# Kernel optimization log

Hardware: AMD Instinct MI355X
Metric: run time of the kernel (lower is better)

Reference implementation:

```python
import jax, jax.numpy as jnp
import numpy as np

DN = ('NCHW', 'OIHW', 'NCHW')

def conv(x, w, b=None, pad=0):
    y = jax.lax.conv_general_dilated(x, w, (1, 1), [(pad, pad), (pad, pad)], dimension_numbers=DN)
    if b is not None:
        y = y + b[None, :, None, None]
    return y

def bn(x, g, b):
    # inference-mode BatchNorm with running_mean=0, running_var=1 (affine only)
    return g[None, :, None, None] * x + b[None, :, None, None]

def gru(msg, h, wg, bg, wc, g, be):
    gates = conv(jnp.concatenate([msg, h], axis=1), wg, bg)  # [B,2,H,W]
    r = jax.nn.sigmoid(gates[:, 0:1])
    u = jax.nn.sigmoid(gates[:, 1:2])
    cnm = jax.nn.leaky_relu(bn(conv(jnp.concatenate([msg, r * h], axis=1), wc), g, be), 0.01)
    return (1.0 - u) * h + u * cnm

def setup_inputs() -> dict:
    key = jax.random.key(0)
    ks = jax.random.split(key, 32)
    B, C, H, W = 8, 10, 192, 192
    s = 0.1
    inp = {
        'f_nodes': jax.random.normal(ks[0], (2, B, C, H, W), jnp.float32),
        'h_nodes': jax.random.normal(ks[1], (3, B, C, H, W), jnp.float32),
        'p_nodes': jax.random.normal(ks[2], (7, B, C, H, W), jnp.float32),
        'xh': jax.random.normal(ks[3], (B, C, H, W), jnp.float32),
        # Decomp_att: 1x1 conv 30->3
        'w_dmap': jax.random.normal(ks[4], (3, 30, 1, 1)) * s,
        'b_dmap': jnp.zeros((3,)),
        # Decomposition relation (shared across 2 children): 3x3 conv 20->10 + BN
        'w_decomp': jax.random.normal(ks[5], (10, 20, 3, 3)) * s,
        'g_decomp': jnp.ones((10,)), 'be_decomp': jnp.zeros((10,)),
        # Comp_att upper: 1x1 conv 40->1 ; lower: 20->1
        'w_cau': jax.random.normal(ks[6], (1, 40, 1, 1)) * s, 'b_cau': jnp.zeros((1,)),
        'w_cal': jax.random.normal(ks[7], (1, 20, 1, 1)) * s, 'b_cal': jnp.zeros((1,)),
        # Composition relation (shared across parts): 3x3 conv 20->10 + BN
        'w_cu': jax.random.normal(ks[8], (10, 20, 3, 3)) * s,
        'g_cu': jnp.ones((10,)), 'be_cu': jnp.zeros((10,)),
        'w_cl': jax.random.normal(ks[9], (10, 20, 3, 3)) * s,
        'g_cl': jnp.ones((10,)), 'be_cl': jnp.zeros((10,)),
        # ConvGRU upper: gates 1x1 20->2, candidate 1x1 20->10 + ABN(leaky_relu)
        'wg_u': jax.random.normal(ks[10], (2, 20, 1, 1)) * s, 'bg_u': jnp.zeros((2,)),
        'wc_u': jax.random.normal(ks[11], (10, 20, 1, 1)) * s,
        'g_u': jnp.ones((10,)), 'be_u': jnp.zeros((10,)),
        # ConvGRU lower
        'wg_l': jax.random.normal(ks[12], (2, 20, 1, 1)) * s, 'bg_l': jnp.zeros((2,)),
        'wc_l': jax.random.normal(ks[13], (10, 20, 1, 1)) * s,
        'g_l': jnp.ones((10,)), 'be_l': jnp.zeros((10,)),
    }
    return inp

def reference(f_nodes, h_nodes, p_nodes, xh,
              w_dmap, b_dmap, w_decomp, g_decomp, be_decomp,
              w_cau, b_cau, w_cal, b_cal,
              w_cu, g_cu, be_cu, w_cl, g_cl, be_cl,
              wg_u, bg_u, wc_u, g_u, be_u,
              wg_l, bg_l, wc_l, g_l, be_l):
    f1 = f_nodes[1]
    h1, h2 = h_nodes[1], h_nodes[2]

    # Decomp_att: 1x1 conv over [f1, h1, h2]
    decomp_map = conv(jnp.concatenate([f1, h1, h2], axis=1), w_dmap, b_dmap)  # [B,3,H,W]
    att = jax.nn.softmax(decomp_map, axis=1)

    # Decomposition (channels 0 is parent-self slot; children use slots 1,2)
    d0 = jax.nn.relu(bn(conv(jnp.concatenate([f1 * att[:, 1:2], h1], axis=1), w_decomp, pad=1), g_decomp, be_decomp))
    d1 = jax.nn.relu(bn(conv(jnp.concatenate([f1 * att[:, 2:3], h2], axis=1), w_decomp, pad=1), g_decomp, be_decomp))

    # Upper half: parts 1..4
    upper = [p_nodes[i] for i in (1, 2, 3, 4)]
    comp_map_u = jax.nn.sigmoid(conv(jnp.concatenate(upper, axis=1), w_cau, b_cau))  # [B,1,H,W]
    comp_u = sum(jax.nn.relu(bn(conv(jnp.concatenate([h1, c * comp_map_u], axis=1), w_cu, pad=1), g_cu, be_cu)) for c in upper)
    msg_u = d0 + comp_u
    xh_u = gru(msg_u, h1, wg_u, bg_u, wc_u, g_u, be_u)

    # Lower half: parts 5..6
    lower = [p_nodes[i] for i in (5, 6)]
    comp_map_l = jax.nn.sigmoid(conv(jnp.concatenate(lower, axis=1), w_cal, b_cal))
    comp_l = sum(jax.nn.relu(bn(conv(jnp.concatenate([h2, c * comp_map_l], axis=1), w_cl, pad=1), g_cl, be_cl)) for c in lower)
    msg_l = d1 + comp_l
    xh_l = gru(msg_l, h2, wg_l, bg_l, wc_l, g_l, be_l)

    xh_new = jnp.stack([h_nodes[0], xh_u, xh_l], axis=0)  # [3,B,10,H,W]
    return (xh_new, decomp_map, comp_map_u, comp_map_l)
```

## Files before the change

### kernel.cpp

```cpp
#include <hip/hip_runtime.h>

#define HW 36864
#define WD 192
#define BB 8
#define CC 10

typedef __attribute__((ext_vector_type(8))) short short8;
typedef __attribute__((ext_vector_type(4))) float f32x4;

__device__ __forceinline__ short f2bf(float v) {
    unsigned u = __float_as_uint(v);
    unsigned r = (u + 0x7fffu + ((u >> 16) & 1u)) >> 16;
    return (short)r;
}

__global__ __launch_bounds__(256) void maps_kernel(
    const float* __restrict__ f_nodes, const float* __restrict__ h_nodes,
    const float* __restrict__ p_nodes,
    const float* __restrict__ w_dmap, const float* __restrict__ b_dmap,
    const float* __restrict__ w_cau, const float* __restrict__ b_cau,
    const float* __restrict__ w_cal, const float* __restrict__ b_cal,
    float* __restrict__ out)
{
    int px = blockIdx.x * 256 + threadIdx.x;
    int b  = px / HW;
    int sp = px - b * HW;

    const float* f1 = f_nodes + (size_t)(1*BB + b)*CC*HW + sp;
    const float* h0 = h_nodes + (size_t)(0*BB + b)*CC*HW + sp;
    const float* h1 = h_nodes + (size_t)(1*BB + b)*CC*HW + sp;
    const float* h2 = h_nodes + (size_t)(2*BB + b)*CC*HW + sp;

    float fv[10], h1v[10], h2v[10];
    #pragma unroll
    for (int c = 0; c < 10; ++c) {
        fv[c]  = f1[(size_t)c*HW];
        h1v[c] = h1[(size_t)c*HW];
        h2v[c] = h2[(size_t)c*HW];
    }

    const size_t O1 = (size_t)3*BB*CC*HW;
    #pragma unroll
    for (int j = 0; j < 3; ++j) {
        float s = b_dmap[j];
        #pragma unroll
        for (int c = 0; c < 10; ++c) s = fmaf(w_dmap[j*30 + c],      fv[c],  s);
        #pragma unroll
        for (int c = 0; c < 10; ++c) s = fmaf(w_dmap[j*30 + 10 + c], h1v[c], s);
        #pragma unroll
        for (int c = 0; c < 10; ++c) s = fmaf(w_dmap[j*30 + 20 + c], h2v[c], s);
        out[O1 + ((size_t)b*3 + j)*HW + sp] = s;
    }

    float su = b_cau[0];
    #pragma unroll
    for (int i = 0; i < 4; ++i) {
        const float* p = p_nodes + (size_t)((1+i)*BB + b)*CC*HW + sp;
        #pragma unroll
        for (int c = 0; c < 10; ++c) su = fmaf(w_cau[i*10 + c], p[(size_t)c*HW], su);
    }
    const size_t O2 = O1 + (size_t)BB*3*HW;
    out[O2 + (size_t)b*HW + sp] = 1.f / (1.f + expf(-su));

    float sl = b_cal[0];
    #pragma unroll
    for (int i = 0; i < 2; ++i) {
        const float* p = p_nodes + (size_t)((5+i)*BB + b)*CC*HW + sp;
        #pragma unroll
        for (int c = 0; c < 10; ++c) sl = fmaf(w_cal[i*10 + c], p[(size_t)c*HW], sl);
    }
    const size_t O3 = O2 + (size_t)BB*HW;
    out[O3 + (size_t)b*HW + sp] = 1.f / (1.f + expf(-sl));

    float* o0 = out + (size_t)b*CC*HW + sp;
    #pragma unroll
    for (int c = 0; c < 10; ++c) o0[(size_t)c*HW] = h0[(size_t)c*HW];
}

__global__ __launch_bounds__(256) void half_kernel(
    const float* __restrict__ f1base,
    const float* __restrict__ hbase,
    const float* __restrict__ pbase, int nparts,
    const float* __restrict__ dmap, int attIdx,
    const float* __restrict__ cmap,
    const float* __restrict__ w_dec,
    const float* __restrict__ gD, const float* __restrict__ bD,
    const float* __restrict__ w_cmp,
    const float* __restrict__ gC, const float* __restrict__ bC,
    const float* __restrict__ wg, const float* __restrict__ bg,
    const float* __restrict__ wc, const float* __restrict__ gG,
    const float* __restrict__ beG,
    float* __restrict__ outp)
{
    __shared__ short sT[342*24];
    __shared__ short sWb[2*16*232];
    __shared__ float sMap[324];
    __shared__ float sMsg[256*12];
    __shared__ float sPar[302];

    const int tid  = threadIdx.x;
    const int lane = tid & 63;
    const int w    = tid >> 6;
    const int g    = lane >> 4;
    const int n    = lane & 15;
    const int b    = blockIdx.z;
    const int x0   = blockIdx.x*16, y0 = blockIdx.y*16;

    {
        int* z = (int*)sT;
        for (int i = tid; i < 342*24/2; i += 256) z[i] = 0;
        int* z2 = (int*)sWb;
        for (int i = tid; i < 2*16*232/2; i += 256) z2[i] = 0;
    }
    __syncthreads();

    for (int i = tid; i < 1800; i += 256) {
        int o = i/180, r = i - o*180;
        int ci = r/9, kp = r - ci*9;
        int slot_d = (ci >= 10) ? (ci - 10) : (ci + 10);
        sWb[o*232 + kp*24 + slot_d]      = f2bf(w_dec[i]);
        sWb[16*232 + o*232 + kp*24 + ci] = f2bf(w_cmp[i]);
    }
    if (tid < 10) {
        sPar[tid]    = gD[tid];  sPar[10+tid] = bD[tid];
        sPar[20+tid] = gC[tid];  sPar[30+tid] = bC[tid];
        sPar[40+tid] = gG[tid];  sPar[50+tid] = beG[tid];
    }
    if (tid < 40) sPar[60+tid]  = wg[tid];
    if (tid < 2)  sPar[100+tid] = bg[tid];
    if (tid >= 56 && tid < 256) sPar[102+(tid-56)] = (tid-56 < 200) ? wc[tid-56] : 0.f;

    for (int r = tid; r < 324; r += 256) {
        int yy = r/18, xx = r - yy*18;
        int gy = y0 + yy - 1, gx = x0 + xx - 1;
        float a = 0.f;
        if ((unsigned)gy < 192u && (unsigned)gx < 192u) {
            const float* dmb = dmap + (size_t)b*3*HW + gy*WD + gx;
            float d0 = dmb[0], d1 = dmb[HW], d2 = dmb[2*HW];
            float mx = fmaxf(d0, fmaxf(d1, d2));
            float e0 = expf(d0-mx), e1 = expf(d1-mx), e2 = expf(d2-mx);
            a = ((attIdx == 1) ? e1 : e2) / (e0 + e1 + e2);
        }
        sMap[r] = a;
    }
    __syncthreads();

    const float* fb = f1base + (size_t)b*CC*HW;
    const float* hb = hbase  + (size_t)b*CC*HW;
    for (int e = tid; e < 3240; e += 256) {
        int c = e/324, r = e - c*324;
        int yy = r/18, xx = r - yy*18;
        int gy = y0 + yy - 1, gx = x0 + xx - 1;
        float vh = 0.f, vf = 0.f;
        if ((unsigned)gy < 192u && (unsigned)gx < 192u) {
            int off = gy*WD + gx;
            vh = hb[(size_t)c*HW + off];
            vf = fb[(size_t)c*HW + off] * sMap[r];
        }
        sT[r*24 + c]      = f2bf(vh);
        sT[r*24 + 10 + c] = f2bf(vf);
    }
    __syncthreads();

    int aoff[7];
    #pragma unroll
    for (int t = 0; t < 7; ++t) {
        int ks = 32*t + 8*g;
        int kp = ks/24;
        int c8 = ks - kp*24;
        int ky = kp/3, kx = kp - ky*3;
        aoff[t] = ((ky*18) + kx + n)*24 + c8;
    }
    const int wbase = w*4*432;

    f32x4 msgf[4];
    {
        short8 bfr[7];
        #pragma unroll
        for (int t = 0; t < 7; ++t)
            bfr[t] = *(const short8*)(sWb + n*232 + 32*t + 8*g);
        f32x4 acc[4];
        #pragma unroll
        for (int mt = 0; mt < 4; ++mt) acc[mt] = (f32x4){0.f,0.f,0.f,0.f};
        #pragma unroll
        for (int t = 0; t < 7; ++t) {
            #pragma unroll
            for (int mt = 0; mt < 4; ++mt) {
                short8 a = *(const short8*)(sT + wbase + mt*432 + aoff[t]);
                acc[mt] = __builtin_amdgcn_mfma_f32_16x16x32_bf16(a, bfr[t], acc[mt], 0, 0, 0);
            }
        }
        int np = (n < 10) ? n : 9;
        float gDv = sPar[np], bDv = sPar[10+np];
        #pragma unroll
        for (int mt = 0; mt < 4; ++mt) {
            #pragma unroll
            for (int j = 0; j < 4; ++j)
                msgf[mt][j] = fmaxf(fmaf(gDv, acc[mt][j], bDv), 0.f);
        }
    }

    for (int r = tid; r < 324; r += 256) {
        int yy = r/18, xx = r - yy*18;
        int gy = y0 + yy - 1, gx = x0 + xx - 1;
        float a = 0.f;
        if ((unsigned)gy < 192u && (unsigned)gx < 192u)
            a = cmap[(size_t)b*HW + gy*WD + gx];
        sMap[r] = a;
    }

    short8 bfc[7];
    #pragma unroll
    for (int t = 0; t < 7; ++t)
        bfc[t] = *(const short8*)(sWb + 16*232 + n*232 + 32*t + 8*g);

    int np = (n < 10) ? n : 9;
    float gCv = sPar[20+np], bCv = sPar[30+np];
    __syncthreads();

    for (int j = 0; j < nparts; ++j) {
        const float* pb = pbase + ((size_t)j*BB + b)*CC*HW;
        for (int e = tid; e < 3240; e += 256) {
            int c = e/324, r = e - c*324;
            int yy = r/18, xx = r - yy*18;
            int gy = y0 + yy - 1, gx = x0 + xx - 1;
            float v = 0.f;
            if ((unsigned)gy < 192u && (unsigned)gx < 192u)
                v = pb[(size_t)c*HW + gy*WD + gx] * sMap[r];
            sT[r*24 + 10 + c] = f2bf(v);
        }
        __syncthreads();

        f32x4 acc[4];
        #pragma unroll
        for (int mt = 0; mt < 4; ++mt) acc[mt] = (f32x4){0.f,0.f,0.f,0.f};
        #pragma unroll
        for (int t = 0; t < 7; ++t) {
            #pragma unroll
            for (int mt = 0; mt < 4; ++mt) {
                short8 a = *(const short8*)(sT + wbase + mt*432 + aoff[t]);
                acc[mt] = __builtin_amdgcn_mfma_f32_16x16x32_bf16(a, bfc[t], acc[mt], 0, 0, 0);
            }
        }
        #pragma unroll
        for (int mt = 0; mt < 4; ++mt) {
            #pragma unroll
            for (int jj = 0; jj < 4; ++jj)
                msgf[mt][jj] += fmaxf(fmaf(gCv, acc[mt][jj], bCv), 0.f);
        }
        __syncthreads();
    }

    if (n < 10) {
        #pragma unroll
        for (int mt = 0; mt < 4; ++mt) {
            #pragma unroll
            for (int r2 = 0; r2 < 4; ++r2) {
                int q = (4*w + mt)*16 + 4*g + r2;
                sMsg[q*12 + n] = msgf[mt][r2];
            }
        }
    }
    __syncthreads();

    {
        int q = tid;
        int row = q >> 4, xx = q & 15;
        int gy = y0 + row, gx = x0 + xx;

        float msg[10], hc[10];
        #pragma unroll
        for (int c = 0; c < 10; ++c) msg[c] = sMsg[q*12 + c];
        const float* hp = hb + gy*WD + gx;
        #pragma unroll
        for (int c = 0; c < 10; ++c) hc[c] = hp[(size_t)c*HW];

        float g0 = sPar[100], g1 = sPar[101];
        #pragma unroll
        for (int c = 0; c < 10; ++c) {
            g0 = fmaf(sPar[60+c], msg[c], g0);
            g1 = fmaf(sPar[80+c], msg[c], g1);
        }
        #pragma unroll
        for (int c = 0; c < 10; ++c) {
            g0 = fmaf(sPar[70+c], hc[c], g0);
            g1 = fmaf(sPar[90+c], hc[c], g1);
        }
        float r = 1.f / (1.f + expf(-g0));
        float u = 1.f / (1.f + expf(-g1));

        float* op = outp + (size_t)b*CC*HW + gy*WD + gx;
        #pragma unroll
        for (int o = 0; o < 10; ++o) {
            float s = 0.f;
            const float* wr = &sPar[102 + o*20];
            #pragma unroll
            for (int c = 0; c < 10; ++c) s = fmaf(wr[c], msg[c], s);
            #pragma unroll
            for (int c = 0; c < 10; ++c) s = fmaf(wr[10+c], r*hc[c], s);
            s = fmaf(sPar[40+o], s, sPar[50+o]);
            s = (s > 0.f) ? s : 0.01f*s;
            op[(size_t)o*HW] = (1.f - u)*hc[o] + u*s;
        }
    }
}

extern "C" void kernel_launch(void* const* d_in, const int* in_sizes, int n_in,
                              void* d_out, int out_size, void* d_ws, size_t ws_size,
                              hipStream_t stream)
{
    const float* f_nodes = (const float*)d_in[0];
    const float* h_nodes = (const float*)d_in[1];
    const float* p_nodes = (const float*)d_in[2];
    const float* w_dmap   = (const float*)d_in[4];
    const float* b_dmap   = (const float*)d_in[5];
    const float* w_decomp = (const float*)d_in[6];
    const float* g_decomp = (const float*)d_in[7];
    const float* be_decomp= (const float*)d_in[8];
    const float* w_cau    = (const float*)d_in[9];
    const float* b_cau    = (const float*)d_in[10];
    const float* w_cal    = (const float*)d_in[11];
    const float* b_cal    = (const float*)d_in[12];
    const float* w_cu     = (const float*)d_in[13];
    const float* g_cu     = (const float*)d_in[14];
    const float* be_cu    = (const float*)d_in[15];
    const float* w_cl     = (const float*)d_in[16];
    const float* g_cl     = (const float*)d_in[17];
    const float* be_cl    = (const float*)d_in[18];
    const float* wg_u     = (const float*)d_in[19];
    const float* bg_u     = (const float*)d_in[20];
    const float* wc_u     = (const float*)d_in[21];
    const float* g_u      = (const float*)d_in[22];
    const float* be_u     = (const float*)d_in[23];
    const float* wg_l     = (const float*)d_in[24];
    const float* bg_l     = (const float*)d_in[25];
    const float* wc_l     = (const float*)d_in[26];
    const float* g_l      = (const float*)d_in[27];
    const float* be_l     = (const float*)d_in[28];

    float* out = (float*)d_out;
    const size_t O1 = (size_t)3*BB*CC*HW;
    const size_t O2 = O1 + (size_t)BB*3*HW;
    const size_t O3 = O2 + (size_t)BB*HW;

    maps_kernel<<<dim3((BB*HW)/256), dim3(256), 0, stream>>>(
        f_nodes, h_nodes, p_nodes, w_dmap, b_dmap, w_cau, b_cau, w_cal, b_cal, out);

    dim3 grid(WD/16, WD/16, BB), blk(256, 1, 1);

    half_kernel<<<grid, blk, 0, stream>>>(
        f_nodes + (size_t)1*BB*CC*HW,
        h_nodes + (size_t)1*BB*CC*HW,
        p_nodes + (size_t)1*BB*CC*HW, 4,
        out + O1, 1, out + O2,
        w_decomp, g_decomp, be_decomp,
        w_cu, g_cu, be_cu,
        wg_u, bg_u, wc_u, g_u, be_u,
        out + (size_t)1*BB*CC*HW);

    half_kernel<<<grid, blk, 0, stream>>>(
        f_nodes + (size_t)1*BB*CC*HW,
        h_nodes + (size_t)2*BB*CC*HW,
        p_nodes + (size_t)5*BB*CC*HW, 2,
        out + O1, 2, out + O3,
        w_decomp, g_decomp, be_decomp,
        w_cl, g_cl, be_cl,
        wg_l, bg_l, wc_l, g_l, be_l,
        out + (size_t)2*BB*CC*HW);
}
```

Baseline: 371.8 us.

## Precompute padded bf16 channel-last workspace and async-DMA tiles into merged half kernel

A prep kernel now computes the attention maps and the softmax/sigmoid scaling. It writes h, the scaled f and the scaled part tensors into a zero-padded bf16 channel-last workspace with 16-channel pixels. The half kernel serves both halves in one launch and loads its tiles with global_load_lds async copies, double-buffering the part tiles. Because the conv is linear, the h-branch of the composition conv is computed once and reused across parts, and the GRU reads h from LDS. The aim is to remove strided fp32 gathers, repeated halo conversion and redundant MFMA work. The cost is extra workspace write/read traffic and GRU inputs rounded to bf16.

```diff
diff --git a/kernel.cpp b/kernel.cpp
--- a/kernel.cpp
+++ b/kernel.cpp
@@ -4,6 +4,9 @@
 #define WD 192
 #define BB 8
 #define CC 10
+#define PW 194
+#define PB ((size_t)(PW*PW*16))
+#define PA ((size_t)BB*PB)
 
 typedef __attribute__((ext_vector_type(8))) short short8;
 typedef __attribute__((ext_vector_type(4))) float f32x4;
@@ -13,89 +16,157 @@
     unsigned r = (u + 0x7fffu + ((u >> 16) & 1u)) >> 16;
     return (short)r;
 }
-
-__global__ __launch_bounds__(256) void maps_kernel(
+__device__ __forceinline__ float b2f(short s) {
+    return __uint_as_float(((unsigned)(unsigned short)s) << 16);
+}
+
+#define ASYNC16(gp, lp) __builtin_amdgcn_global_load_lds( \
+    (const __attribute__((address_space(1))) void*)(gp),  \
+    (__attribute__((address_space(3))) void*)(lp), 16, 0, 0)
+
+__device__ __forceinline__ void store16(short* d, const float* v, float s) {
+    short8 lo, hi;
+    #pragma unroll
+    for (int i = 0; i < 8; ++i) lo[i] = f2bf(v[i]*s);
+    hi = (short8){f2bf(v[8]*s), f2bf(v[9]*s), 0,0,0,0,0,0};
+    *(short8*)d = lo;
+    *(short8*)(d+8) = hi;
+}
+
+__global__ __launch_bounds__(256) void prep_kernel(
     const float* __restrict__ f_nodes, const float* __restrict__ h_nodes,
     const float* __restrict__ p_nodes,
     const float* __restrict__ w_dmap, const float* __restrict__ b_dmap,
     const float* __restrict__ w_cau, const float* __restrict__ b_cau,
     const float* __restrict__ w_cal, const float* __restrict__ b_cal,
+    float* __restrict__ out, short* __restrict__ ws)
+{
+    int t = blockIdx.x*256 + threadIdx.x;
+    if (t >= BB*PW*PW) return;
+    int b  = t / (PW*PW);
+    int pp = t - b*(PW*PW);
+    int py = pp / PW, px = pp - py*PW;
+    short* wb = ws + (size_t)b*PB + (size_t)pp*16;
+
+    if (py == 0 || py == PW-1 || px == 0 || px == PW-1) {
+        short8 z = (short8){0,0,0,0,0,0,0,0};
+        #pragma unroll
+        for (int a = 0; a < 10; ++a) {
+            *(short8*)(wb + (size_t)a*PA)     = z;
+            *(short8*)(wb + (size_t)a*PA + 8) = z;
+        }
+        return;
+    }
+    int sp = (py-1)*WD + (px-1);
+
+    const float* f1 = f_nodes + ((size_t)(BB   + b))*CC*HW + sp;
+    const float* h0 = h_nodes + ((size_t)(       b))*CC*HW + sp;
+    const float* h1 = h_nodes + ((size_t)(BB   + b))*CC*HW + sp;
+    const float* h2 = h_nodes + ((size_t)(2*BB + b))*CC*HW + sp;
+
+    float fv[10], av[10], bv[10];
+    #pragma unroll
+    for (int c = 0; c < 10; ++c) {
+        fv[c] = f1[(size_t)c*HW];
+        av[c] = h1[(size_t)c*HW];
+        bv[c] = h2[(size_t)c*HW];
+    }
+
+    const size_t O1 = (size_t)3*BB*CC*HW;
+    const size_t O2 = O1 + (size_t)BB*3*HW;
+    const size_t O3 = O2 + (size_t)BB*HW;
+
+    float dm[3];
+    #pragma unroll
+    for (int j = 0; j < 3; ++j) {
+        float s = b_dmap[j];
+        #pragma unroll
+        for (int c = 0; c < 10; ++c) s = fmaf(w_dmap[j*30 + c],      fv[c], s);
+        #pragma unroll
+        for (int c = 0; c < 10; ++c) s = fmaf(w_dmap[j*30 + 10 + c], av[c], s);
+        #pragma unroll
+        for (int c = 0; c < 10; ++c) s = fmaf(w_dmap[j*30 + 20 + c], bv[c], s);
+        dm[j] = s;
+        out[O1 + ((size_t)b*3 + j)*HW + sp] = s;
+    }
+    float mx = fmaxf(dm[0], fmaxf(dm[1], dm[2]));
+    float e0 = expf(dm[0]-mx), e1 = expf(dm[1]-mx), e2 = expf(dm[2]-mx);
+    float inv = 1.f / (e0 + e1 + e2);
+    float a1 = e1*inv, a2 = e2*inv;
+
+    store16(wb + 0*PA, av, 1.f);
+    store16(wb + 1*PA, bv, 1.f);
+    store16(wb + 2*PA, fv, a1);
+    store16(wb + 3*PA, fv, a2);
+
+    float* o0 = out + (size_t)b*CC*HW + sp;
+    #pragma unroll
+    for (int c = 0; c < 10; ++c) o0[(size_t)c*HW] = h0[(size_t)c*HW];
+
+    {
+        float pv[4][10];
+        float su = b_cau[0];
+        #pragma unroll
+        for (int i = 0; i < 4; ++i) {
+            const float* p = p_nodes + ((size_t)((1+i)*BB + b))*CC*HW + sp;
+            #pragma unroll
+            for (int c = 0; c < 10; ++c) pv[i][c] = p[(size_t)c*HW];
+            #pragma unroll
+            for (int c = 0; c < 10; ++c) su = fmaf(w_cau[i*10 + c], pv[i][c], su);
+        }
+        float cmU = 1.f / (1.f + expf(-su));
+        out[O2 + (size_t)b*HW + sp] = cmU;
+        #pragma unroll
+        for (int i = 0; i < 4; ++i) store16(wb + (size_t)(4+i)*PA, pv[i], cmU);
+    }
+    {
+        float qv[2][10];
+        float sl = b_cal[0];
+        #pragma unroll
+        for (int i = 0; i < 2; ++i) {
+            const float* p = p_nodes + ((size_t)((5+i)*BB + b))*CC*HW + sp;
+            #pragma unroll
+            for (int c = 0; c < 10; ++c) qv[i][c] = p[(size_t)c*HW];
+            #pragma unroll
+            for (int c = 0; c < 10; ++c) sl = fmaf(w_cal[i*10 + c], qv[i][c], sl);
+        }
+        float cmL = 1.f / (1.f + expf(-sl));
+        out[O3 + (size_t)b*HW + sp] = cmL;
+        #pragma unroll
+        for (int i = 0; i < 2; ++i) store16(wb + (size_t)(8+i)*PA, qv[i], cmL);
+    }
+}
+
+__device__ __forceinline__ void dma_tile(short* lds, const short* g,
+                                         int tid, int y0, int x0)
+{
+    #pragma unroll
+    for (int r = 0; r < 3; ++r) {
+        int idx = r*256 + tid;
+        int row = idx / 36;
+        int col = idx - row*36;
+        size_t go = (idx < 648) ? (((size_t)(y0+row)*PW + x0)*16 + (size_t)col*8)
+                                : (size_t)0;
+        ASYNC16(g + go, lds + (size_t)idx*8);
+    }
+}
+
+__global__ __launch_bounds__(256) void half_kernel(
+    const short* __restrict__ ws,
+    const float* __restrict__ w_dec, const float* __restrict__ gD, const float* __restrict__ bD,
+    const float* __restrict__ w_cu, const float* __restrict__ gCu, const float* __restrict__ bCu,
+    const float* __restrict__ w_cl, const float* __restrict__ gCl, const float* __restrict__ bCl,
+    const float* __restrict__ wg_u, const float* __restrict__ bg_u, const float* __restrict__ wc_u,
+    const float* __restrict__ g_u, const float* __restrict__ be_u,
+    const float* __restrict__ wg_l, const float* __restrict__ bg_l, const float* __restrict__ wc_l,
+    const float* __restrict__ g_l, const float* __restrict__ be_l,
     float* __restrict__ out)
 {
-    int px = blockIdx.x * 256 + threadIdx.x;
-    int b  = px / HW;
-    int sp = px - b * HW;
-
-    const float* f1 = f_nodes + (size_t)(1*BB + b)*CC*HW + sp;
-    const float* h0 = h_nodes + (size_t)(0*BB + b)*CC*HW + sp;
-    const float* h1 = h_nodes + (size_t)(1*BB + b)*CC*HW + sp;
-    const float* h2 = h_nodes + (size_t)(2*BB + b)*CC*HW + sp;
-
-    float fv[10], h1v[10], h2v[10];
-    #pragma unroll
-    for (int c = 0; c < 10; ++c) {
-        fv[c]  = f1[(size_t)c*HW];
-        h1v[c] = h1[(size_t)c*HW];
-        h2v[c] = h2[(size_t)c*HW];
-    }
-
-    const size_t O1 = (size_t)3*BB*CC*HW;
-    #pragma unroll
-    for (int j = 0; j < 3; ++j) {
-        float s = b_dmap[j];
-        #pragma unroll
-        for (int c = 0; c < 10; ++c) s = fmaf(w_dmap[j*30 + c],      fv[c],  s);
-        #pragma unroll
-        for (int c = 0; c < 10; ++c) s = fmaf(w_dmap[j*30 + 10 + c], h1v[c], s);
-        #pragma unroll
-        for (int c = 0; c < 10; ++c) s = fmaf(w_dmap[j*30 + 20 + c], h2v[c], s);
-        out[O1 + ((size_t)b*3 + j)*HW + sp] = s;
-    }
-
-    float su = b_cau[0];
-    #pragma unroll
-    for (int i = 0; i < 4; ++i) {
-        const float* p = p_nodes + (size_t)((1+i)*BB + b)*CC*HW + sp;
-        #pragma unroll
-        for (int c = 0; c < 10; ++c) su = fmaf(w_cau[i*10 + c], p[(size_t)c*HW], su);
-    }
-    const size_t O2 = O1 + (size_t)BB*3*HW;
-    out[O2 + (size_t)b*HW + sp] = 1.f / (1.f + expf(-su));
-
-    float sl = b_cal[0];
-    #pragma unroll
-    for (int i = 0; i < 2; ++i) {
-        const float* p = p_nodes + (size_t)((5+i)*BB + b)*CC*HW + sp;
-        #pragma unroll
-        for (int c = 0; c < 10; ++c) sl = fmaf(w_cal[i*10 + c], p[(size_t)c*HW], sl);
-    }
-    const size_t O3 = O2 + (size_t)BB*HW;
-    out[O3 + (size_t)b*HW + sp] = 1.f / (1.f + expf(-sl));
-
-    float* o0 = out + (size_t)b*CC*HW + sp;
-    #pragma unroll
-    for (int c = 0; c < 10; ++c) o0[(size_t)c*HW] = h0[(size_t)c*HW];
-}
-
-__global__ __launch_bounds__(256) void half_kernel(
-    const float* __restrict__ f1base,
-    const float* __restrict__ hbase,
-    const float* __restrict__ pbase, int nparts,
-    const float* __restrict__ dmap, int attIdx,
-    const float* __restrict__ cmap,
-    const float* __restrict__ w_dec,
-    const float* __restrict__ gD, const float* __restrict__ bD,
-    const float* __restrict__ w_cmp,
-    const float* __restrict__ gC, const float* __restrict__ bC,
-    const float* __restrict__ wg, const float* __restrict__ bg,
-    const float* __restrict__ wc, const float* __restrict__ gG,
-    const float* __restrict__ beG,
-    float* __restrict__ outp)
-{
-    __shared__ short sT[342*24];
-    __shared__ short sWb[2*16*232];
-    __shared__ float sMap[324];
-    __shared__ float sMsg[256*12];
+    __shared__ __align__(16) short sTh[6144];
+    __shared__ __align__(16) short sTp0[6144];
+    __shared__ __align__(16) short sTp1[6144];
+    __shared__ __align__(16) short sWb[4*2688];
+    __shared__ float sMsg[256*13];
     __shared__ float sPar[302];
 
     const int tid  = threadIdx.x;
@@ -103,23 +174,36 @@
     const int w    = tid >> 6;
     const int g    = lane >> 4;
     const int n    = lane & 15;
-    const int b    = blockIdx.z;
+    const int half = blockIdx.z >> 3;
+    const int b    = blockIdx.z & 7;
     const int x0   = blockIdx.x*16, y0 = blockIdx.y*16;
 
-    {
-        int* z = (int*)sT;
-        for (int i = tid; i < 342*24/2; i += 256) z[i] = 0;
-        int* z2 = (int*)sWb;
-        for (int i = tid; i < 2*16*232/2; i += 256) z2[i] = 0;
-    }
+    const float* w_cmp = half ? w_cl : w_cu;
+    const float* gC  = half ? gCl  : gCu;
+    const float* bC  = half ? bCl  : bCu;
+    const float* wg  = half ? wg_l : wg_u;
+    const float* bg  = half ? bg_l : bg_u;
+    const float* wc  = half ? wc_l : wc_u;
+    const float* gG  = half ? g_l  : g_u;
+    const float* beG = half ? be_l : be_u;
+    const int nparts = half ? 2 : 4;
+
+    const short* hArr  = ws + (size_t)half*PA     + (size_t)b*PB;
+    const short* fArr  = ws + (size_t)(2+half)*PA + (size_t)b*PB;
+    const short* pArr0 = ws + (size_t)(4+half*4)*PA + (size_t)b*PB;
+
+    for (int i = tid; i < 4*2688/2; i += 256) ((int*)sWb)[i] = 0;
+    dma_tile(sTh,  hArr,  tid, y0, x0);
+    dma_tile(sTp0, fArr,  tid, y0, x0);
+    dma_tile(sTp1, pArr0, tid, y0, x0);
     __syncthreads();
 
     for (int i = tid; i < 1800; i += 256) {
-        int o = i/180, r = i - o*180;
-        int ci = r/9, kp = r - ci*9;
-        int slot_d = (ci >= 10) ? (ci - 10) : (ci + 10);
-        sWb[o*232 + kp*24 + slot_d]      = f2bf(w_dec[i]);
-        sWb[16*232 + o*232 + kp*24 + ci] = f2bf(w_cmp[i]);
+        int o = i/180, r = i - o*180, ci = r/9, kp = r - ci*9;
+        int c  = (ci < 10) ? ci : ci - 10;
+        int s2 = (ci < 10) ? 0 : 1;
+        sWb[s2*2688     + o*168 + kp*16 + c] = f2bf(w_dec[i]);
+        sWb[(2+s2)*2688 + o*168 + kp*16 + c] = f2bf(w_cmp[i]);
     }
     if (tid < 10) {
         sPar[tid]    = gD[tid];  sPar[10+tid] = bD[tid];
@@ -129,151 +213,100 @@
     if (tid < 40) sPar[60+tid]  = wg[tid];
     if (tid < 2)  sPar[100+tid] = bg[tid];
     if (tid >= 56 && tid < 256) sPar[102+(tid-56)] = (tid-56 < 200) ? wc[tid-56] : 0.f;
-
-    for (int r = tid; r < 324; r += 256) {
-        int yy = r/18, xx = r - yy*18;
-        int gy = y0 + yy - 1, gx = x0 + xx - 1;
-        float a = 0.f;
-        if ((unsigned)gy < 192u && (unsigned)gx < 192u) {
-            const float* dmb = dmap + (size_t)b*3*HW + gy*WD + gx;
-            float d0 = dmb[0], d1 = dmb[HW], d2 = dmb[2*HW];
-            float mx = fmaxf(d0, fmaxf(d1, d2));
-            float e0 = expf(d0-mx), e1 = expf(d1-mx), e2 = expf(d2-mx);
-            a = ((attIdx == 1) ? e1 : e2) / (e0 + e1 + e2);
-        }
-        sMap[r] = a;
-    }
     __syncthreads();
 
-    const float* fb = f1base + (size_t)b*CC*HW;
-    const float* hb = hbase  + (size_t)b*CC*HW;
-    for (int e = tid; e < 3240; e += 256) {
-        int c = e/324, r = e - c*324;
-        int yy = r/18, xx = r - yy*18;
-        int gy = y0 + yy - 1, gx = x0 + xx - 1;
-        float vh = 0.f, vf = 0.f;
-        if ((unsigned)gy < 192u && (unsigned)gx < 192u) {
-            int off = gy*WD + gx;
-            vh = hb[(size_t)c*HW + off];
-            vf = fb[(size_t)c*HW + off] * sMap[r];
-        }
-        sT[r*24 + c]      = f2bf(vh);
-        sT[r*24 + 10 + c] = f2bf(vf);
-    }
+    int aoff[5];
+    #pragma unroll
+    for (int t5 = 0; t5 < 5; ++t5) {
+        int k  = 32*t5 + 8*g;
+        int kp = k >> 4;
+        int c8 = k & 15;
+        if (kp < 9) { int ky = kp/3, kx = kp - ky*3; aoff[t5] = (ky*18 + kx + n)*16 + c8; }
+        else        aoff[t5] = 0;
+    }
+    const int wbase = w*4*288;
+
+    short8 bF[5], bH[5], bCh[5], bCp[5];
+    #pragma unroll
+    for (int t5 = 0; t5 < 5; ++t5) {
+        int ko = 32*t5 + 8*g;
+        bF[t5]  = *(const short8*)(sWb + 0*2688 + n*168 + ko);
+        bH[t5]  = *(const short8*)(sWb + 1*2688 + n*168 + ko);
+        bCh[t5] = *(const short8*)(sWb + 2*2688 + n*168 + ko);
+        bCp[t5] = *(const short8*)(sWb + 3*2688 + n*168 + ko);
+    }
+
+    f32x4 accD[4], accH[4];
+    #pragma unroll
+    for (int mt = 0; mt < 4; ++mt) { accD[mt] = (f32x4){0,0,0,0}; accH[mt] = (f32x4){0,0,0,0}; }
+    #pragma unroll
+    for (int t5 = 0; t5 < 5; ++t5) {
+        #pragma unroll
+        for (int mt = 0; mt < 4; ++mt) {
+            short8 a = *(const short8*)(sTp0 + wbase + mt*288 + aoff[t5]);
+            accD[mt] = __builtin_amdgcn_mfma_f32_16x16x32_bf16(a, bF[t5], accD[mt], 0,0,0);
+        }
+    }
+    #pragma unroll
+    for (int t5 = 0; t5 < 5; ++t5) {
+        #pragma unroll
+        for (int mt = 0; mt < 4; ++mt) {
+            short8 a = *(const short8*)(sTh + wbase + mt*288 + aoff[t5]);
+            accD[mt] = __builtin_amdgcn_mfma_f32_16x16x32_bf16(a, bH[t5],  accD[mt], 0,0,0);
+            accH[mt] = __builtin_amdgcn_mfma_f32_16x16x32_bf16(a, bCh[t5], accH[mt], 0,0,0);
+        }
+    }
+    const int np = (n < 10) ? n : 9;
+    const float gDv = sPar[np],    bDv = sPar[10+np];
+    const float gCv = sPar[20+np], bCv = sPar[30+np];
+    f32x4 msgf[4];
+    #pragma unroll
+    for (int mt = 0; mt < 4; ++mt)
+        #pragma unroll
+        for (int j = 0; j < 4; ++j)
+            msgf[mt][j] = fmaxf(fmaf(gDv, accD[mt][j], bDv), 0.f);
     __syncthreads();
 
-    int aoff[7];
-    #pragma unroll
-    for (int t = 0; t < 7; ++t) {
-        int ks = 32*t + 8*g;
-        int kp = ks/24;
-        int c8 = ks - kp*24;
-        int ky = kp/3, kx = kp - ky*3;
-        aoff[t] = ((ky*18) + kx + n)*24 + c8;
-    }
-    const int wbase = w*4*432;
-
-    f32x4 msgf[4];
+    for (int j = 0; j < nparts; ++j) {
+        if (j+1 < nparts)
+            dma_tile((j&1) ? sTp1 : sTp0, pArr0 + (size_t)(j+1)*PA, tid, y0, x0);
+        const short* cur = (j&1) ? sTp0 : sTp1;
+        f32x4 acc[4];
+        #pragma unroll
+        for (int mt = 0; mt < 4; ++mt) acc[mt] = (f32x4){0,0,0,0};
+        #pragma unroll
+        for (int t5 = 0; t5 < 5; ++t5) {
+            #pragma unroll
+            for (int mt = 0; mt < 4; ++mt) {
+                short8 a = *(const short8*)(cur + wbase + mt*288 + aoff[t5]);
+                acc[mt] = __builtin_amdgcn_mfma_f32_16x16x32_bf16(a, bCp[t5], acc[mt], 0,0,0);
+            }
+        }
+        #pragma unroll
+        for (int mt = 0; mt < 4; ++mt)
+            #pragma unroll
+            for (int jj = 0; jj < 4; ++jj)
+                msgf[mt][jj] += fmaxf(fmaf(gCv, accH[mt][jj] + acc[mt][jj], bCv), 0.f);
+        __syncthreads();
+    }
+
+    if (n < 10) {
+        #pragma unroll
+        for (int mt = 0; mt < 4; ++mt)
+            #pragma unroll
+            for (int r2 = 0; r2 < 4; ++r2)
+                sMsg[((4*w + mt)*16 + 4*g + r2)*13 + n] = msgf[mt][r2];
+    }
+    __syncthreads();
+
     {
-        short8 bfr[7];
-        #pragma unroll
-        for (int t = 0; t < 7; ++t)
-            bfr[t] = *(const short8*)(sWb + n*232 + 32*t + 8*g);
-        f32x4 acc[4];
-        #pragma unroll
-        for (int mt = 0; mt < 4; ++mt) acc[mt] = (f32x4){0.f,0.f,0.f,0.f};
-        #pragma unroll
-        for (int t = 0; t < 7; ++t) {
-            #pragma unroll
-            for (int mt = 0; mt < 4; ++mt) {
-                short8 a = *(const short8*)(sT + wbase + mt*432 + aoff[t]);
-                acc[mt] = __builtin_amdgcn_mfma_f32_16x16x32_bf16(a, bfr[t], acc[mt], 0, 0, 0);
-            }
-        }
-        int np = (n < 10) ? n : 9;
-        float gDv = sPar[np], bDv = sPar[10+np];
-        #pragma unroll
-        for (int mt = 0; mt < 4; ++mt) {
-            #pragma unroll
-            for (int j = 0; j < 4; ++j)
-                msgf[mt][j] = fmaxf(fmaf(gDv, acc[mt][j], bDv), 0.f);
-        }
-    }
-
-    for (int r = tid; r < 324; r += 256) {
-        int yy = r/18, xx = r - yy*18;
-        int gy = y0 + yy - 1, gx = x0 + xx - 1;
-        float a = 0.f;
-        if ((unsigned)gy < 192u && (unsigned)gx < 192u)
-            a = cmap[(size_t)b*HW + gy*WD + gx];
-        sMap[r] = a;
-    }
-
-    short8 bfc[7];
-    #pragma unroll
-    for (int t = 0; t < 7; ++t)
-        bfc[t] = *(const short8*)(sWb + 16*232 + n*232 + 32*t + 8*g);
-
-    int np = (n < 10) ? n : 9;
-    float gCv = sPar[20+np], bCv = sPar[30+np];
-    __syncthreads();
-
-    for (int j = 0; j < nparts; ++j) {
-        const float* pb = pbase + ((size_t)j*BB + b)*CC*HW;
-        for (int e = tid; e < 3240; e += 256) {
-            int c = e/324, r = e - c*324;
-            int yy = r/18, xx = r - yy*18;
-            int gy = y0 + yy - 1, gx = x0 + xx - 1;
-            float v = 0.f;
-            if ((unsigned)gy < 192u && (unsigned)gx < 192u)
-                v = pb[(size_t)c*HW + gy*WD + gx] * sMap[r];
-            sT[r*24 + 10 + c] = f2bf(v);
-        }
-        __syncthreads();
-
-        f32x4 acc[4];
-        #pragma unroll
-        for (int mt = 0; mt < 4; ++mt) acc[mt] = (f32x4){0.f,0.f,0.f,0.f};
-        #pragma unroll
-        for (int t = 0; t < 7; ++t) {
-            #pragma unroll
-            for (int mt = 0; mt < 4; ++mt) {
-                short8 a = *(const short8*)(sT + wbase + mt*432 + aoff[t]);
-                acc[mt] = __builtin_amdgcn_mfma_f32_16x16x32_bf16(a, bfc[t], acc[mt], 0, 0, 0);
-            }
-        }
-        #pragma unroll
-        for (int mt = 0; mt < 4; ++mt) {
-            #pragma unroll
-            for (int jj = 0; jj < 4; ++jj)
-                msgf[mt][jj] += fmaxf(fmaf(gCv, acc[mt][jj], bCv), 0.f);
-        }
-        __syncthreads();
-    }
-
-    if (n < 10) {
-        #pragma unroll
-        for (int mt = 0; mt < 4; ++mt) {
-            #pragma unroll
-            for (int r2 = 0; r2 < 4; ++r2) {
-                int q = (4*w + mt)*16 + 4*g + r2;
-                sMsg[q*12 + n] = msgf[mt][r2];
-            }
-        }
-    }
-    __syncthreads();
-
-    {
-        int q = tid;
-        int row = q >> 4, xx = q & 15;
+        int row = tid >> 4, xx = tid & 15;
         int gy = y0 + row, gx = x0 + xx;
-
         float msg[10], hc[10];
         #pragma unroll
-        for (int c = 0; c < 10; ++c) msg[c] = sMsg[q*12 + c];
-        const float* hp = hb + gy*WD + gx;
-        #pragma unroll
-        for (int c = 0; c < 10; ++c) hc[c] = hp[(size_t)c*HW];
+        for (int c = 0; c < 10; ++c) msg[c] = sMsg[tid*13 + c];
+        #pragma unroll
+        for (int c = 0; c < 10; ++c) hc[c] = b2f(sTh[((row+1)*18 + (xx+1))*16 + c]);
 
         float g0 = sPar[100], g1 = sPar[101];
         #pragma unroll
@@ -289,7 +322,7 @@
         float r = 1.f / (1.f + expf(-g0));
         float u = 1.f / (1.f + expf(-g1));
 
-        float* op = outp + (size_t)b*CC*HW + gy*WD + gx;
+        float* op = out + (size_t)(1+half)*BB*CC*HW + (size_t)b*CC*HW + gy*WD + gx;
         #pragma unroll
         for (int o = 0; o < 10; ++o) {
             float s = 0.f;
@@ -339,32 +372,16 @@
     const float* be_l     = (const float*)d_in[28];
 
     float* out = (float*)d_out;
-    const size_t O1 = (size_t)3*BB*CC*HW;
-    const size_t O2 = O1 + (size_t)BB*3*HW;
-    const size_t O3 = O2 + (size_t)BB*HW;
-
-    maps_kernel<<<dim3((BB*HW)/256), dim3(256), 0, stream>>>(
-        f_nodes, h_nodes, p_nodes, w_dmap, b_dmap, w_cau, b_cau, w_cal, b_cal, out);
-
-    dim3 grid(WD/16, WD/16, BB), blk(256, 1, 1);
-
-    half_kernel<<<grid, blk, 0, stream>>>(
-        f_nodes + (size_t)1*BB*CC*HW,
-        h_nodes + (size_t)1*BB*CC*HW,
-        p_nodes + (size_t)1*BB*CC*HW, 4,
-        out + O1, 1, out + O2,
-        w_decomp, g_decomp, be_decomp,
-        w_cu, g_cu, be_cu,
+    short* ws  = (short*)d_ws;
+
+    prep_kernel<<<dim3((BB*PW*PW + 255)/256), dim3(256), 0, stream>>>(
+        f_nodes, h_nodes, p_nodes, w_dmap, b_dmap,
+        w_cau, b_cau, w_cal, b_cal, out, ws);
+
+    half_kernel<<<dim3(WD/16, WD/16, 16), dim3(256), 0, stream>>>(
+        ws, w_decomp, g_decomp, be_decomp,
+        w_cu, g_cu, be_cu, w_cl, g_cl, be_cl,
         wg_u, bg_u, wc_u, g_u, be_u,
-        out + (size_t)1*BB*CC*HW);
-
-    half_kernel<<<grid, blk, 0, stream>>>(
-        f_nodes + (size_t)1*BB*CC*HW,
-        h_nodes + (size_t)2*BB*CC*HW,
-        p_nodes + (size_t)5*BB*CC*HW, 2,
-        out + O1, 2, out + O3,
-        w_decomp, g_decomp, be_decomp,
-        w_cl, g_cl, be_cl,
         wg_l, bg_l, wc_l, g_l, be_l,
-        out + (size_t)2*BB*CC*HW);
-}
+        out);
+}
```

Measured after the change: 317.3 us. -14.6%, faster.
